# Optimization experiments

Measured on AMD Instinct MI355X. Metric: run time of the kernel, lower is better.

## Reference

```python
import jax, jax.numpy as jnp
import numpy as np

N = 50000      # nodes
E = 200000     # edges
F_IN = 128     # input features
H = 1024       # hidden
C = 16         # classes
K = 3          # TAGConv hops
EPS = 1e-5


def setup_inputs() -> dict:
    key = jax.random.key(0)
    ks = jax.random.split(key, 12)
    s = 0.02
    x = jax.random.normal(ks[0], (N, F_IN), jnp.float32)
    edge_index = jax.random.randint(ks[1], (2, E), 0, N, dtype=jnp.int64)
    weight = jax.random.uniform(ks[2], (E,), jnp.float32)
    return {
        "x": x,
        "edge_index": edge_index,
        "weight": weight,
        "W1": jax.random.normal(ks[3], (K + 1, F_IN, H), jnp.float32) * s,
        "b1": jnp.zeros((H,), jnp.float32),
        "g1": jnp.ones((H,), jnp.float32),
        "be1": jnp.zeros((H,), jnp.float32),
        "a1": jnp.ones((H,), jnp.float32),
        "W2": jax.random.normal(ks[4], (K + 1, H, H), jnp.float32) * s,
        "b2": jnp.zeros((H,), jnp.float32),
        "g2": jnp.ones((H,), jnp.float32),
        "be2": jnp.zeros((H,), jnp.float32),
        "a2": jnp.ones((H,), jnp.float32),
        "W3": jax.random.normal(ks[5], (K + 1, H, C), jnp.float32) * s,
        "b3": jnp.zeros((C,), jnp.float32),
    }


def _edge_norm(weight, src, dst):
    # gcn_norm without self-loops: deg from edge weights at target nodes
    deg = jax.ops.segment_sum(weight, dst, num_segments=N)
    safe = jnp.where(deg > 0, deg, 1.0)
    dinv = jnp.where(deg > 0, jax.lax.rsqrt(safe), 0.0)
    norm_w = dinv[src] * weight * dinv[dst]
    cnt = jax.ops.segment_sum(jnp.ones((E,), weight.dtype), dst, num_segments=N)
    cnt_inv = jnp.where(cnt > 0, 1.0 / jnp.where(cnt > 0, cnt, 1.0), 0.0)
    return norm_w, cnt_inv


def _tagconv(x, W, b, src, dst, norm_w, cnt_inv):
    # out = sum_k lin_k(x_k), x_k = mean-aggr of norm_w * x_{k-1}[src] at dst
    out = x @ W[0]
    h = x
    for k in range(1, K + 1):
        msg = norm_w[:, None] * h[src]                       # [E, d]
        h = jax.ops.segment_sum(msg, dst, num_segments=N) * cnt_inv[:, None]
        out = out + h @ W[k]
    return out + b


def _graphnorm(x, g, be, a):
    # single graph: per-graph stats = global stats over nodes
    mean = jnp.mean(x, axis=0)
    out = x - a * mean
    var = jnp.mean(out * out, axis=0)
    return g * out / jnp.sqrt(var + EPS) + be


def reference(x, edge_index, weight, W1, b1, g1, be1, a1,
              W2, b2, g2, be2, a2, W3, b3):
    src, dst = edge_index[0], edge_index[1]
    norm_w, cnt_inv = _edge_norm(weight, src, dst)
    h = jax.nn.elu(_tagconv(x, W1, b1, src, dst, norm_w, cnt_inv))
    h = _graphnorm(h, g1, be1, a1)
    h = jax.nn.elu(_tagconv(h, W2, b2, src, dst, norm_w, cnt_inv))
    h = _graphnorm(h, g2, be2, a2)
    return _tagconv(h, W3, b3, src, dst, norm_w, cnt_inv)
```

## Files before the change

kernel.cpp:

```cpp
#include <hip/hip_runtime.h>
#include <hip/hip_bf16.h>
#include <math.h>

#define N_NODES 50000
#define N_EDGES 200000
#define FIN 128
#define HID 1024
#define NCLS 16
#define EPSN 1e-5f
#define NPAD 50048
#define MT 391
#define EPITCH 136

typedef __attribute__((ext_vector_type(8))) short short8;
typedef __attribute__((ext_vector_type(8))) unsigned short ushort8;
typedef __attribute__((ext_vector_type(4))) unsigned short u16x4;
typedef __attribute__((ext_vector_type(4))) float f32x4;

static __device__ __forceinline__ float bf2f(unsigned short u) {
  union { unsigned int i; float f; } v; v.i = ((unsigned int)u) << 16; return v.f;
}
static __device__ __forceinline__ unsigned short f2bf(float f) {
  __hip_bfloat16 h = __float2bfloat16(f);
  return *(unsigned short*)&h;
}

#define ASYNC16(gsrc, ldst)                                                   \
  __builtin_amdgcn_global_load_lds(                                           \
      (const __attribute__((address_space(1))) void*)(gsrc),                  \
      (__attribute__((address_space(3))) void*)(ldst), 16, 0, 0)


__global__ __launch_bounds__(256) void k_deg_cnt(const int* __restrict__ dst,
                                                 const float* __restrict__ w,
                                                 float* deg, int* cnt) {
  int e = blockIdx.x * 256 + threadIdx.x;
  if (e < N_EDGES) {
    int d = dst[e];
    atomicAdd(&deg[d], w[e]);
    atomicAdd(&cnt[d], 1);
  }
}

__global__ __launch_bounds__(256) void k_normw(const int* __restrict__ src,
                                               const int* __restrict__ dst,
                                               const float* __restrict__ w,
                                               const float* __restrict__ deg,
                                               float* __restrict__ normw) {
  int e = blockIdx.x * 256 + threadIdx.x;
  if (e < N_EDGES) {
    float ds = deg[src[e]], dd = deg[dst[e]];
    float a = ds > 0.f ? rsqrtf(ds) : 0.f;
    float b = dd > 0.f ? rsqrtf(dd) : 0.f;
    normw[e] = a * w[e] * b;
  }
}

__global__ __launch_bounds__(256) void k_cntinv(const int* __restrict__ cnt,
                                                float* __restrict__ cnt_inv) {
  int n = blockIdx.x * 256 + threadIdx.x;
  if (n < N_NODES) {
    int c = cnt[n];
    cnt_inv[n] = c > 0 ? 1.f / (float)c : 0.f;
  }
}

__global__ __launch_bounds__(1024) void k_scan_a(const int* __restrict__ cnt,
                                                 int* __restrict__ rowptr,
                                                 int* __restrict__ bsums) {
  __shared__ int sm[1024];
  int tid = threadIdx.x;
  int i = blockIdx.x * 1024 + tid;
  int v = (i < N_NODES) ? cnt[i] : 0;
  sm[tid] = v;
  __syncthreads();
  for (int off = 1; off < 1024; off <<= 1) {
    int t = (tid >= off) ? sm[tid - off] : 0;
    __syncthreads();
    sm[tid] += t;
    __syncthreads();
  }
  if (i < N_NODES) rowptr[i] = sm[tid] - v;
  if (tid == 1023) bsums[blockIdx.x] = sm[1023];
}

__global__ void k_scan_b(int* bsums, int nb) {
  if (threadIdx.x == 0 && blockIdx.x == 0) {
    int s = 0;
    for (int i = 0; i < nb; ++i) { int t = bsums[i]; bsums[i] = s; s += t; }
  }
}

__global__ __launch_bounds__(1024) void k_scan_c(int* __restrict__ rowptr,
                                                 const int* __restrict__ bsums) {
  int i = blockIdx.x * 1024 + threadIdx.x;
  if (i < N_NODES) rowptr[i] += bsums[blockIdx.x];
}

__global__ __launch_bounds__(256) void k_fill(const int* __restrict__ src,
                                              const int* __restrict__ dst,
                                              const float* __restrict__ normw,
                                              const int* __restrict__ rowptr,
                                              int* __restrict__ fill,
                                              int* __restrict__ csr_src,
                                              float* __restrict__ csr_w) {
  int e = blockIdx.x * 256 + threadIdx.x;
  if (e < N_EDGES) {
    int d = dst[e];
    int pos = rowptr[d] + atomicAdd(&fill[d], 1);
    csr_src[pos] = src[e];
    csr_w[pos] = normw[e];
  }
}


__global__ void k_transpose_bf16(const float* __restrict__ in,
                                 __hip_bfloat16* __restrict__ out, int K, int N) {
  __shared__ float tile[32][33];
  int kb = blockIdx.x * 32, nb = blockIdx.y * 32;
  int tx = threadIdx.x, ty = threadIdx.y;
  for (int i = ty; i < 32; i += 8) tile[i][tx] = in[(size_t)(kb + i) * N + nb + tx];
  __syncthreads();
  for (int i = ty; i < 32; i += 8)
    out[(size_t)(nb + i) * K + kb + tx] = __float2bfloat16(tile[tx][i]);
}

__global__ __launch_bounds__(256) void k_packw3(const float* __restrict__ W3,
                                                __hip_bfloat16* __restrict__ W3T) {
  int idx = blockIdx.x * 256 + threadIdx.x;
  if (idx < 4 * 1024 * 16) {
    int k3 = idx >> 14, r = idx & 16383, k = r >> 4, j = r & 15;
    W3T[(size_t)(k3 * 16 + j) * 1024 + k] = __float2bfloat16(W3[idx]);
  }
}

__global__ __launch_bounds__(256) void k_x_to_bf16(const float* __restrict__ x,
                                                   unsigned short* __restrict__ xc) {
  int i = blockIdx.x * 256 + threadIdx.x;
  if (i < N_NODES * FIN / 4) {
    int n = i >> 5, c4 = i & 31;
    const float4 v = ((const float4*)x)[i];
    u16x4 o;
    o[0] = f2bf(v.x); o[1] = f2bf(v.y); o[2] = f2bf(v.z); o[3] = f2bf(v.w);
    *(u16x4*)&xc[(size_t)n * 512 + c4 * 4] = o;
  }
}


template <int W>
__global__ __launch_bounds__(256) void k_spmm_v(
    const unsigned short* __restrict__ src_t, int sp,
    unsigned short* __restrict__ dst_t, int dp,
    const int* __restrict__ rowptr, const int* __restrict__ cnt,
    const float* __restrict__ cnt_inv,
    const int* __restrict__ csr_src,
    const float* __restrict__ csr_w) {
  constexpr int G = W / 8;
  int gl = blockIdx.x * 256 + threadIdx.x;
  int node = gl / G;
  if (node >= N_NODES) return;
  int fl = (gl % G) * 8;
  int beg = rowptr[node], ne = cnt[node];
  float acc[8] = {0.f, 0.f, 0.f, 0.f, 0.f, 0.f, 0.f, 0.f};
  for (int i = 0; i < ne; ++i) {
    int s = csr_src[beg + i];
    float wt = csr_w[beg + i];
    ushort8 v = *(const ushort8*)&src_t[(size_t)s * sp + fl];
#pragma unroll
    for (int j = 0; j < 8; ++j) acc[j] += wt * bf2f(v[j]);
  }
  float ci = cnt_inv[node];
  ushort8 o;
#pragma unroll
  for (int j = 0; j < 8; ++j) o[j] = f2bf(acc[j] * ci);
  *(ushort8*)&dst_t[(size_t)node * dp + fl] = o;
}

__global__ __launch_bounds__(256) void k_spmm16(const float* __restrict__ src_t, int sp,
                                                const float* __restrict__ addend, int ap,
                                                const float* __restrict__ b3,
                                                float* __restrict__ out, int op,
                                                const int* __restrict__ rowptr,
                                                const int* __restrict__ cnt,
                                                const float* __restrict__ cnt_inv,
                                                const int* __restrict__ csr_src,
                                                const float* __restrict__ csr_w) {
  int idx = blockIdx.x * 256 + threadIdx.x;
  if (idx >= N_NODES * 16) return;
  int node = idx >> 4, f = idx & 15;
  int beg = rowptr[node], ne = cnt[node];
  float acc = 0.f;
  for (int i = 0; i < ne; ++i)
    acc += csr_w[beg + i] * src_t[(size_t)csr_src[beg + i] * sp + f];
  float r = acc * cnt_inv[node] + addend[(size_t)node * ap + f];
  if (b3) r += b3[f];
  out[(size_t)node * op + f] = r;
}


__global__ __launch_bounds__(256, 4) void k_gemm(
    const unsigned short* __restrict__ A, int lda,
    const unsigned short* __restrict__ BT, int ldb,
    const unsigned short* __restrict__ Cinit, int ldci,
    void* __restrict__ Cout, int ldc, int cbf16,
    int M, int Nout, int K,
    const float* __restrict__ bias, int do_elu) {
  __shared__ __align__(16) unsigned short smem[128 * EPITCH];
  int tid = threadIdx.x;
  int wave = tid >> 6, lane = tid & 63;
  int wm = wave >> 1, wn = wave & 1;
  int l15 = lane & 15, quad = lane >> 4;
  int im = blockIdx.y, in_ = blockIdx.x;

  f32x4 acc[4][4];
  if (Cinit) {
    {
      int r = tid >> 1, hf = tid & 1;
      const unsigned short* gsrc =
          &Cinit[(size_t)(im * 128 + r) * ldci + in_ * 128 + hf * 64];
#pragma unroll
      for (int v = 0; v < 8; ++v)
        *(ushort8*)&smem[r * EPITCH + hf * 64 + v * 8] = *(const ushort8*)&gsrc[v * 8];
    }
    __syncthreads();
#pragma unroll
    for (int i = 0; i < 4; ++i)
#pragma unroll
      for (int j = 0; j < 4; ++j)
#pragma unroll
        for (int reg = 0; reg < 4; ++reg)
          acc[i][j][reg] =
              bf2f(smem[(wm * 64 + i * 16 + quad * 4 + reg) * EPITCH + wn * 64 + j * 16 + l15]);
    __syncthreads();
  } else {
#pragma unroll
    for (int i = 0; i < 4; ++i)
#pragma unroll
      for (int j = 0; j < 4; ++j) acc[i][j] = (f32x4){0.f, 0.f, 0.f, 0.f};
  }

  int srow = tid >> 2;
  int sl = (tid & 3) ^ (srow & 3) ^ ((srow >> 2) & 3);
  const unsigned short* gA0 = &A[(size_t)(im * 128 + srow) * lda + sl * 8];
  const unsigned short* gA1 = &A[(size_t)(im * 128 + 64 + srow) * lda + sl * 8];
  const unsigned short* gB0 = &BT[(size_t)(in_ * 128 + srow) * ldb + sl * 8];
  const unsigned short* gB1 = &BT[(size_t)(in_ * 128 + 64 + srow) * ldb + sl * 8];
  unsigned short* ldsA = smem;
  unsigned short* ldsB = smem + 8192;
  int woff0 = (wave * 64) * 8;
  int woff1 = (256 + wave * 64) * 8;
  int rsl = (quad ^ (l15 & 3) ^ (l15 >> 2)) * 8;

  auto stage = [&](int k0, int p) {
    ASYNC16(gA0 + k0, &ldsA[p * 4096 + woff0]);
    ASYNC16(gA1 + k0, &ldsA[p * 4096 + woff1]);
    ASYNC16(gB0 + k0, &ldsB[p * 4096 + woff0]);
    ASYNC16(gB1 + k0, &ldsB[p * 4096 + woff1]);
  };
  auto compute = [&](int p) {
    short8 af[4], bf[4];
#pragma unroll
    for (int i = 0; i < 4; ++i)
      af[i] = *(const short8*)&ldsA[p * 4096 + (wm * 64 + i * 16 + l15) * 32 + rsl];
#pragma unroll
    for (int j = 0; j < 4; ++j)
      bf[j] = *(const short8*)&ldsB[p * 4096 + (wn * 64 + j * 16 + l15) * 32 + rsl];
#pragma unroll
    for (int i = 0; i < 4; ++i)
#pragma unroll
      for (int j = 0; j < 4; ++j)
        acc[i][j] = __builtin_amdgcn_mfma_f32_16x16x32_bf16(af[i], bf[j], acc[i][j], 0, 0, 0);
  };

  stage(0, 0);
  __syncthreads();
  int p = 0;
  for (int k0 = 32; k0 < K; k0 += 32) {
    stage(k0, p ^ 1);
    compute(p);
    __syncthreads();
    p ^= 1;
  }
  compute(p);
  __syncthreads();

  if (cbf16) {
#pragma unroll
    for (int i = 0; i < 4; ++i)
#pragma unroll
      for (int j = 0; j < 4; ++j) {
        int cg = in_ * 128 + wn * 64 + j * 16 + l15;
        float bv = bias ? bias[cg] : 0.f;
#pragma unroll
        for (int reg = 0; reg < 4; ++reg) {
          float v = acc[i][j][reg] + bv;
          if (do_elu) v = v > 0.f ? v : expm1f(v);
          smem[(wm * 64 + i * 16 + quad * 4 + reg) * EPITCH + wn * 64 + j * 16 + l15] = f2bf(v);
        }
      }
    __syncthreads();
    int r = tid >> 1, hf = tid & 1;
    unsigned short* gdst =
        (unsigned short*)Cout + (size_t)(im * 128 + r) * ldc + in_ * 128 + hf * 64;
#pragma unroll
    for (int v = 0; v < 8; ++v)
      *(ushort8*)&gdst[v * 8] = *(const ushort8*)&smem[r * EPITCH + hf * 64 + v * 8];
  } else {
#pragma unroll
    for (int i = 0; i < 4; ++i) {
      int r0 = im * 128 + wm * 64 + i * 16 + quad * 4;
#pragma unroll
      for (int j = 0; j < 4; ++j) {
        int c = in_ * 128 + wn * 64 + j * 16 + l15;
        if (c < Nout) {
#pragma unroll
          for (int reg = 0; reg < 4; ++reg) {
            int r = r0 + reg;
            if (r < M) {
              float v = acc[i][j][reg];
              if (bias) v += bias[c];
              if (do_elu) v = v > 0.f ? v : expm1f(v);
              ((float*)Cout)[(size_t)r * ldc + c] = v;
            }
          }
        }
      }
    }
  }
}


__global__ __launch_bounds__(128) void k_colstats(const unsigned short* __restrict__ h,
                                                  float* __restrict__ stats) {
  int f0 = threadIdx.x * 8;
  int r0 = blockIdx.y * 128;
  int r1 = r0 + 128; if (r1 > N_NODES) r1 = N_NODES;
  float s[8] = {0,0,0,0,0,0,0,0}, s2[8] = {0,0,0,0,0,0,0,0};
  for (int r = r0; r < r1; ++r) {
    ushort8 v = *(const ushort8*)&h[(size_t)r * HID + f0];
#pragma unroll
    for (int j = 0; j < 8; ++j) { float x = bf2f(v[j]); s[j] += x; s2[j] += x * x; }
  }
#pragma unroll
  for (int j = 0; j < 8; ++j) {
    atomicAdd(&stats[f0 + j], s[j]);
    atomicAdd(&stats[HID + f0 + j], s2[j]);
  }
}

__global__ __launch_bounds__(256) void k_finalize(const float* __restrict__ g,
                                                  const float* __restrict__ be,
                                                  const float* __restrict__ a,
                                                  float* __restrict__ stats) {
  int f = blockIdx.x * 256 + threadIdx.x;
  if (f < HID) {
    float m = stats[f] / (float)N_NODES;
    float ex2 = stats[HID + f] / (float)N_NODES;
    float av = a[f];
    float var = ex2 - 2.f * av * m * m + av * av * m * m;
    float alpha = g[f] * rsqrtf(var + EPSN);
    stats[2 * HID + f] = alpha;
    stats[3 * HID + f] = be[f] - alpha * av * m;
  }
}

__global__ __launch_bounds__(256) void k_normalize(unsigned short* __restrict__ h,
                                                   const float* __restrict__ stats) {
  int i = blockIdx.x * 256 + threadIdx.x;
  if (i < N_NODES * HID / 8) {
    int f0 = (i * 8) & 1023;
    ushort8 v = *(ushort8*)&h[(size_t)i * 8];
#pragma unroll
    for (int j = 0; j < 8; ++j)
      v[j] = f2bf(stats[2 * HID + f0 + j] * bf2f(v[j]) + stats[3 * HID + f0 + j]);
    *(ushort8*)&h[(size_t)i * 8] = v;
  }
}


extern "C" void kernel_launch(void* const* d_in, const int* in_sizes, int n_in,
                              void* d_out, int out_size, void* d_ws, size_t ws_size,
                              hipStream_t stream) {
  const float* x   = (const float*)d_in[0];
  const int*   ei  = (const int*)d_in[1];
  const float* w   = (const float*)d_in[2];
  const float* W1  = (const float*)d_in[3];
  const float* b1  = (const float*)d_in[4];
  const float* g1  = (const float*)d_in[5];
  const float* be1 = (const float*)d_in[6];
  const float* a1  = (const float*)d_in[7];
  const float* W2  = (const float*)d_in[8];
  const float* b2  = (const float*)d_in[9];
  const float* g2  = (const float*)d_in[10];
  const float* be2 = (const float*)d_in[11];
  const float* a2  = (const float*)d_in[12];
  const float* W3  = (const float*)d_in[13];
  const float* b3  = (const float*)d_in[14];
  float* out = (float*)d_out;

  const int* srcI = ei;
  const int* dstI = ei + N_EDGES;

  char* base = (char*)d_ws;
  size_t off = 0;
  auto alloc = [&](size_t bytes) -> char* {
    char* p = base + off;
    off += (bytes + 255) & ~(size_t)255;
    return p;
  };

  float* deg      = (float*)alloc(N_NODES * 4);
  int*   cnt      = (int*)alloc(N_NODES * 4);
  float* cnt_inv  = (float*)alloc(N_NODES * 4);
  float* normw    = (float*)alloc(N_EDGES * 4);
  int*   rowptr   = (int*)alloc((N_NODES + 1) * 4);
  int*   fill     = (int*)alloc(N_NODES * 4);
  int*   bsums    = (int*)alloc(64 * 4);
  int*   csr_src  = (int*)alloc(N_EDGES * 4);
  float* csr_w    = (float*)alloc(N_EDGES * 4);
  float* stats    = (float*)alloc(4 * HID * 4);
  __hip_bfloat16* W1T = (__hip_bfloat16*)alloc((size_t)1024 * 512 * 2);
  __hip_bfloat16* W2T = (__hip_bfloat16*)alloc((size_t)1024 * 4096 * 2);
  __hip_bfloat16* W3T = (__hip_bfloat16*)alloc((size_t)128 * 1024 * 2);
  const size_t FT = (size_t)NPAD * HID * 2;
  unsigned short* T0 = (unsigned short*)alloc(FT);
  unsigned short* T1 = (unsigned short*)alloc(FT);
  size_t rem = (ws_size > off) ? (ws_size - off) : 0;
  bool full = rem >= FT + 1024;
  unsigned short *T2 = nullptr, *Q = nullptr, *R = nullptr;
  int wcols = 0;
  if (full) {
    T2 = (unsigned short*)alloc(FT);
  } else {
    wcols = 512;
    if (rem < 2 * (size_t)NPAD * 512 * 2 + 1024) wcols = 256;
    if (wcols == 256 && rem < 2 * (size_t)NPAD * 256 * 2 + 1024) wcols = 128;
    Q = (unsigned short*)alloc((size_t)NPAD * wcols * 2);
    R = (unsigned short*)alloc((size_t)NPAD * wcols * 2);
  }
  float* Z  = (float*)T0;
  float* t0 = (float*)((char*)T0 + (size_t)16 * 1024 * 1024);
  float* t1 = (float*)((char*)T0 + (size_t)24 * 1024 * 1024);
  (void)n_in; (void)in_sizes; (void)out_size;

  const int EB = (N_EDGES + 255) / 256;
  const int NB = (N_NODES + 255) / 256;

  (void)hipMemsetAsync(deg, 0, N_NODES * 4, stream);
  (void)hipMemsetAsync(cnt, 0, N_NODES * 4, stream);
  (void)hipMemsetAsync(fill, 0, N_NODES * 4, stream);
  k_deg_cnt<<<EB, 256, 0, stream>>>(dstI, w, deg, cnt);
  k_normw<<<EB, 256, 0, stream>>>(srcI, dstI, w, deg, normw);
  k_cntinv<<<NB, 256, 0, stream>>>(cnt, cnt_inv);
  k_scan_a<<<49, 1024, 0, stream>>>(cnt, rowptr, bsums);
  k_scan_b<<<1, 64, 0, stream>>>(bsums, 49);
  k_scan_c<<<49, 1024, 0, stream>>>(rowptr, bsums);
  k_fill<<<EB, 256, 0, stream>>>(srcI, dstI, normw, rowptr, fill, csr_src, csr_w);

  k_transpose_bf16<<<dim3(512 / 32, 1024 / 32), dim3(32, 8), 0, stream>>>(W1, W1T, 512, 1024);
  k_transpose_bf16<<<dim3(4096 / 32, 1024 / 32), dim3(32, 8), 0, stream>>>(W2, W2T, 4096, 1024);
  k_packw3<<<(65536 + 255) / 256, 256, 0, stream>>>(W3, W3T);

  const unsigned short* W2Tu = (const unsigned short*)W2T;

  k_x_to_bf16<<<(N_NODES * FIN / 4 + 255) / 256, 256, 0, stream>>>(x, T1);
  {
    int blocks = (N_NODES * 16 + 255) / 256;
    for (int k = 1; k <= 3; ++k)
      k_spmm_v<128><<<blocks, 256, 0, stream>>>(
          T1 + (k - 1) * FIN, 512, T1 + k * FIN, 512,
          rowptr, cnt, cnt_inv, csr_src, csr_w);
  }
  k_gemm<<<dim3(8, MT), 256, 0, stream>>>(
      T1, 512, (const unsigned short*)W1T, 512,
      nullptr, 0, T0, HID, 1, N_NODES, HID, 512, b1, 1);
  (void)hipMemsetAsync(stats, 0, 2 * HID * 4, stream);
  k_colstats<<<dim3(1, MT), 128, 0, stream>>>(T0, stats);
  k_finalize<<<4, 256, 0, stream>>>(g1, be1, a1, stats);
  k_normalize<<<(N_NODES * HID / 8) / 256, 256, 0, stream>>>(T0, stats);

  if (full) {
    const int SPB = (N_NODES * 128 + 255) / 256;
    k_gemm<<<dim3(8, MT), 256, 0, stream>>>(
        T0, 1024, W2Tu + 3 * 1024, 4096,
        nullptr, 0, T1, 1024, 1, N_NODES, 1024, 1024, nullptr, 0);
    k_spmm_v<1024><<<SPB, 256, 0, stream>>>(T1, 1024, T2, 1024,
                                            rowptr, cnt, cnt_inv, csr_src, csr_w);
    k_gemm<<<dim3(8, MT), 256, 0, stream>>>(
        T0, 1024, W2Tu + 2 * 1024, 4096,
        T2, 1024, T1, 1024, 1, N_NODES, 1024, 1024, nullptr, 0);
    k_spmm_v<1024><<<SPB, 256, 0, stream>>>(T1, 1024, T2, 1024,
                                            rowptr, cnt, cnt_inv, csr_src, csr_w);
    k_gemm<<<dim3(8, MT), 256, 0, stream>>>(
        T0, 1024, W2Tu + 1 * 1024, 4096,
        T2, 1024, T1, 1024, 1, N_NODES, 1024, 1024, nullptr, 0);
    k_spmm_v<1024><<<SPB, 256, 0, stream>>>(T1, 1024, T2, 1024,
                                            rowptr, cnt, cnt_inv, csr_src, csr_w);
    k_gemm<<<dim3(8, MT), 256, 0, stream>>>(
        T0, 1024, W2Tu + 0 * 1024, 4096,
        T2, 1024, T1, 1024, 1, N_NODES, 1024, 1024, b2, 1);
  } else {
    auto spmm_w = [&](const unsigned short* s, unsigned short* d) {
      int blocks = (N_NODES * (wcols / 8) + 255) / 256;
      if (wcols == 512)
        k_spmm_v<512><<<blocks, 256, 0, stream>>>(s, wcols, d, wcols,
            rowptr, cnt, cnt_inv, csr_src, csr_w);
      else if (wcols == 256)
        k_spmm_v<256><<<blocks, 256, 0, stream>>>(s, wcols, d, wcols,
            rowptr, cnt, cnt_inv, csr_src, csr_w);
      else
        k_spmm_v<128><<<blocks, 256, 0, stream>>>(s, wcols, d, wcols,
            rowptr, cnt, cnt_inv, csr_src, csr_w);
    };
    for (int c = 0; c < HID; c += wcols) {
      const unsigned short* Wb = W2Tu + (size_t)c * 4096;
      k_gemm<<<dim3(wcols / 128, MT), 256, 0, stream>>>(
          T0, 1024, Wb + 3 * 1024, 4096,
          nullptr, 0, Q, wcols, 1, N_NODES, wcols, 1024, nullptr, 0);
      spmm_w(Q, R);
      k_gemm<<<dim3(wcols / 128, MT), 256, 0, stream>>>(
          T0, 1024, Wb + 2 * 1024, 4096,
          R, wcols, Q, wcols, 1, N_NODES, wcols, 1024, nullptr, 0);
      spmm_w(Q, R);
      k_gemm<<<dim3(wcols / 128, MT), 256, 0, stream>>>(
          T0, 1024, Wb + 1 * 1024, 4096,
          R, wcols, Q, wcols, 1, N_NODES, wcols, 1024, nullptr, 0);
      spmm_w(Q, R);
      k_gemm<<<dim3(wcols / 128, MT), 256, 0, stream>>>(
          T0, 1024, Wb + 0 * 1024, 4096,
          R, wcols, T1 + c, 1024, 1, N_NODES, wcols, 1024, b2 + c, 1);
    }
  }
  (void)hipMemsetAsync(stats, 0, 2 * HID * 4, stream);
  k_colstats<<<dim3(1, MT), 128, 0, stream>>>(T1, stats);
  k_finalize<<<4, 256, 0, stream>>>(g2, be2, a2, stats);
  k_normalize<<<(N_NODES * HID / 8) / 256, 256, 0, stream>>>(T1, stats);

  k_gemm<<<dim3(1, MT), 256, 0, stream>>>(
      T1, 1024, (const unsigned short*)W3T, 1024,
      nullptr, 0, Z, 64, 0, N_NODES, 64, 1024, nullptr, 0);
  const int SB = (N_NODES * 16 + 255) / 256;
  k_spmm16<<<SB, 256, 0, stream>>>(Z + 48, 64, Z + 32, 64, nullptr, t0, 16,
                                   rowptr, cnt, cnt_inv, csr_src, csr_w);
  k_spmm16<<<SB, 256, 0, stream>>>(t0, 16, Z + 16, 64, nullptr, t1, 16,
                                   rowptr, cnt, cnt_inv, csr_src, csr_w);
  k_spmm16<<<SB, 256, 0, stream>>>(t1, 16, Z + 0, 64, b3, out, 16,
                                   rowptr, cnt, cnt_inv, csr_src, csr_w);
}
```

Baseline: 2.107 ms.

## Fold first GraphNorm affine into layer-2 weights and per-hop bias vectors

Drops the explicit normalize pass over the 50000x1024 hidden activations after layer 1. The per-feature GraphNorm scale is folded into the transposed bf16 W2, and the shift is folded into per-hop bias vectors ck computed by a new small kernel, which the GEMM epilogues then add. This is valid because aggregation is linear, but it relies on finalize having written scale and shift into stats at offsets 2*HID and 3*HID. It also packs CSR source index and weight into one int2 array, and makes column statistics reduce through shared memory to cut global atomics.

```diff
diff --git a/kernel.cpp b/kernel.cpp
--- a/kernel.cpp
+++ b/kernel.cpp
@@ -102,14 +102,12 @@
                                               const float* __restrict__ normw,
                                               const int* __restrict__ rowptr,
                                               int* __restrict__ fill,
-                                              int* __restrict__ csr_src,
-                                              float* __restrict__ csr_w) {
+                                              int2* __restrict__ csr_ew) {
   int e = blockIdx.x * 256 + threadIdx.x;
   if (e < N_EDGES) {
     int d = dst[e];
     int pos = rowptr[d] + atomicAdd(&fill[d], 1);
-    csr_src[pos] = src[e];
-    csr_w[pos] = normw[e];
+    csr_ew[pos] = make_int2(src[e], __float_as_int(normw[e]));
   }
 }
 
@@ -125,6 +123,40 @@
     out[(size_t)(nb + i) * K + kb + tx] = __float2bfloat16(tile[tx][i]);
 }
 
+__global__ void k_transpose_scale_bf16(const float* __restrict__ in,
+                                       __hip_bfloat16* __restrict__ out, int K, int N,
+                                       const float* __restrict__ alpha) {
+  __shared__ float tile[32][33];
+  int kb = blockIdx.x * 32, nb = blockIdx.y * 32;
+  int tx = threadIdx.x, ty = threadIdx.y;
+  for (int i = ty; i < 32; i += 8) tile[i][tx] = in[(size_t)(kb + i) * N + nb + tx];
+  __syncthreads();
+  float sc = alpha[(kb + tx) & (HID - 1)];
+  for (int i = ty; i < 32; i += 8)
+    out[(size_t)(nb + i) * K + kb + tx] = __float2bfloat16(tile[tx][i] * sc);
+}
+
+__global__ __launch_bounds__(256) void k_ck(const float* __restrict__ W2,
+                                            const float* __restrict__ beta,
+                                            const float* __restrict__ b2,
+                                            float* __restrict__ ck) {
+  int k3 = blockIdx.x, tid = threadIdx.x;
+  float acc[4] = {0.f, 0.f, 0.f, 0.f};
+  const float* Wk = W2 + (size_t)k3 * HID * HID;
+  for (int in = 0; in < HID; ++in) {
+    float s = beta[in];
+    const float* row = Wk + (size_t)in * HID;
+#pragma unroll
+    for (int j = 0; j < 4; ++j) acc[j] += s * row[tid + j * 256];
+  }
+#pragma unroll
+  for (int j = 0; j < 4; ++j) {
+    float v = acc[j];
+    if (k3 == 0) v += b2[tid + j * 256];
+    ck[k3 * HID + tid + j * 256] = v;
+  }
+}
+
 __global__ __launch_bounds__(256) void k_packw3(const float* __restrict__ W3,
                                                 __hip_bfloat16* __restrict__ W3T) {
   int idx = blockIdx.x * 256 + threadIdx.x;
@@ -153,8 +185,7 @@
     unsigned short* __restrict__ dst_t, int dp,
     const int* __restrict__ rowptr, const int* __restrict__ cnt,
     const float* __restrict__ cnt_inv,
-    const int* __restrict__ csr_src,
-    const float* __restrict__ csr_w) {
+    const int2* __restrict__ csr_ew) {
   constexpr int G = W / 8;
   int gl = blockIdx.x * 256 + threadIdx.x;
   int node = gl / G;
@@ -163,9 +194,9 @@
   int beg = rowptr[node], ne = cnt[node];
   float acc[8] = {0.f, 0.f, 0.f, 0.f, 0.f, 0.f, 0.f, 0.f};
   for (int i = 0; i < ne; ++i) {
-    int s = csr_src[beg + i];
-    float wt = csr_w[beg + i];
-    ushort8 v = *(const ushort8*)&src_t[(size_t)s * sp + fl];
+    int2 e = csr_ew[beg + i];
+    float wt = __int_as_float(e.y);
+    ushort8 v = *(const ushort8*)&src_t[(size_t)e.x * sp + fl];
 #pragma unroll
     for (int j = 0; j < 8; ++j) acc[j] += wt * bf2f(v[j]);
   }
@@ -183,15 +214,16 @@
                                                 const int* __restrict__ rowptr,
                                                 const int* __restrict__ cnt,
                                                 const float* __restrict__ cnt_inv,
-                                                const int* __restrict__ csr_src,
-                                                const float* __restrict__ csr_w) {
+                                                const int2* __restrict__ csr_ew) {
   int idx = blockIdx.x * 256 + threadIdx.x;
   if (idx >= N_NODES * 16) return;
   int node = idx >> 4, f = idx & 15;
   int beg = rowptr[node], ne = cnt[node];
   float acc = 0.f;
-  for (int i = 0; i < ne; ++i)
-    acc += csr_w[beg + i] * src_t[(size_t)csr_src[beg + i] * sp + f];
+  for (int i = 0; i < ne; ++i) {
+    int2 e = csr_ew[beg + i];
+    acc += __int_as_float(e.y) * src_t[(size_t)e.x * sp + f];
+  }
   float r = acc * cnt_inv[node] + addend[(size_t)node * ap + f];
   if (b3) r += b3[f];
   out[(size_t)node * op + f] = r;
@@ -330,11 +362,14 @@
 }
 
 
-__global__ __launch_bounds__(128) void k_colstats(const unsigned short* __restrict__ h,
+__global__ __launch_bounds__(512) void k_colstats(const unsigned short* __restrict__ h,
                                                   float* __restrict__ stats) {
-  int f0 = threadIdx.x * 8;
-  int r0 = blockIdx.y * 128;
-  int r1 = r0 + 128; if (r1 > N_NODES) r1 = N_NODES;
+  __shared__ float sm[4 * 2048];
+  int tid = threadIdx.x;
+  int f0 = (tid & 127) * 8;
+  int q = tid >> 7;
+  int r0 = blockIdx.y * 128 + q * 32;
+  int r1 = r0 + 32; if (r1 > N_NODES) r1 = N_NODES;
   float s[8] = {0,0,0,0,0,0,0,0}, s2[8] = {0,0,0,0,0,0,0,0};
   for (int r = r0; r < r1; ++r) {
     ushort8 v = *(const ushort8*)&h[(size_t)r * HID + f0];
@@ -343,8 +378,13 @@
   }
 #pragma unroll
   for (int j = 0; j < 8; ++j) {
-    atomicAdd(&stats[f0 + j], s[j]);
-    atomicAdd(&stats[HID + f0 + j], s2[j]);
+    sm[q * 2048 + f0 + j] = s[j];
+    sm[q * 2048 + 1024 + f0 + j] = s2[j];
+  }
+  __syncthreads();
+  for (int idx = tid; idx < 2048; idx += 512) {
+    float v = sm[idx] + sm[2048 + idx] + sm[4096 + idx] + sm[6144 + idx];
+    atomicAdd(&stats[idx], v);
   }
 }
 
@@ -416,9 +456,9 @@
   int*   rowptr   = (int*)alloc((N_NODES + 1) * 4);
   int*   fill     = (int*)alloc(N_NODES * 4);
   int*   bsums    = (int*)alloc(64 * 4);
-  int*   csr_src  = (int*)alloc(N_EDGES * 4);
-  float* csr_w    = (float*)alloc(N_EDGES * 4);
+  int2*  csr_ew   = (int2*)alloc((size_t)N_EDGES * 8);
   float* stats    = (float*)alloc(4 * HID * 4);
+  float* ck       = (float*)alloc(4 * HID * 4);
   __hip_bfloat16* W1T = (__hip_bfloat16*)alloc((size_t)1024 * 512 * 2);
   __hip_bfloat16* W2T = (__hip_bfloat16*)alloc((size_t)1024 * 4096 * 2);
   __hip_bfloat16* W3T = (__hip_bfloat16*)alloc((size_t)128 * 1024 * 2);
@@ -455,10 +495,9 @@
   k_scan_a<<<49, 1024, 0, stream>>>(cnt, rowptr, bsums);
   k_scan_b<<<1, 64, 0, stream>>>(bsums, 49);
   k_scan_c<<<49, 1024, 0, stream>>>(rowptr, bsums);
-  k_fill<<<EB, 256, 0, stream>>>(srcI, dstI, normw, rowptr, fill, csr_src, csr_w);
+  k_fill<<<EB, 256, 0, stream>>>(srcI, dstI, normw, rowptr, fill, csr_ew);
 
   k_transpose_bf16<<<dim3(512 / 32, 1024 / 32), dim3(32, 8), 0, stream>>>(W1, W1T, 512, 1024);
-  k_transpose_bf16<<<dim3(4096 / 32, 1024 / 32), dim3(32, 8), 0, stream>>>(W2, W2T, 4096, 1024);
   k_packw3<<<(65536 + 255) / 256, 256, 0, stream>>>(W3, W3T);
 
   const unsigned short* W2Tu = (const unsigned short*)W2T;
@@ -469,70 +508,72 @@
     for (int k = 1; k <= 3; ++k)
       k_spmm_v<128><<<blocks, 256, 0, stream>>>(
           T1 + (k - 1) * FIN, 512, T1 + k * FIN, 512,
-          rowptr, cnt, cnt_inv, csr_src, csr_w);
+          rowptr, cnt, cnt_inv, csr_ew);
   }
   k_gemm<<<dim3(8, MT), 256, 0, stream>>>(
       T1, 512, (const unsigned short*)W1T, 512,
       nullptr, 0, T0, HID, 1, N_NODES, HID, 512, b1, 1);
   (void)hipMemsetAsync(stats, 0, 2 * HID * 4, stream);
-  k_colstats<<<dim3(1, MT), 128, 0, stream>>>(T0, stats);
+  k_colstats<<<dim3(1, MT), 512, 0, stream>>>(T0, stats);
   k_finalize<<<4, 256, 0, stream>>>(g1, be1, a1, stats);
-  k_normalize<<<(N_NODES * HID / 8) / 256, 256, 0, stream>>>(T0, stats);
+  k_transpose_scale_bf16<<<dim3(4096 / 32, 1024 / 32), dim3(32, 8), 0, stream>>>(
+      W2, W2T, 4096, 1024, stats + 2 * HID);
+  k_ck<<<4, 256, 0, stream>>>(W2, stats + 3 * HID, b2, ck);
 
   if (full) {
     const int SPB = (N_NODES * 128 + 255) / 256;
     k_gemm<<<dim3(8, MT), 256, 0, stream>>>(
         T0, 1024, W2Tu + 3 * 1024, 4096,
-        nullptr, 0, T1, 1024, 1, N_NODES, 1024, 1024, nullptr, 0);
+        nullptr, 0, T1, 1024, 1, N_NODES, 1024, 1024, ck + 3 * 1024, 0);
     k_spmm_v<1024><<<SPB, 256, 0, stream>>>(T1, 1024, T2, 1024,
-                                            rowptr, cnt, cnt_inv, csr_src, csr_w);
+                                            rowptr, cnt, cnt_inv, csr_ew);
     k_gemm<<<dim3(8, MT), 256, 0, stream>>>(
         T0, 1024, W2Tu + 2 * 1024, 4096,
-        T2, 1024, T1, 1024, 1, N_NODES, 1024, 1024, nullptr, 0);
+        T2, 1024, T1, 1024, 1, N_NODES, 1024, 1024, ck + 2 * 1024, 0);
     k_spmm_v<1024><<<SPB, 256, 0, stream>>>(T1, 1024, T2, 1024,
-                                            rowptr, cnt, cnt_inv, csr_src, csr_w);
+                                            rowptr, cnt, cnt_inv, csr_ew);
     k_gemm<<<dim3(8, MT), 256, 0, stream>>>(
         T0, 1024, W2Tu + 1 * 1024, 4096,
-        T2, 1024, T1, 1024, 1, N_NODES, 1024, 1024, nullptr, 0);
+        T2, 1024, T1, 1024, 1, N_NODES, 1024, 1024, ck + 1 * 1024, 0);
     k_spmm_v<1024><<<SPB, 256, 0, stream>>>(T1, 1024, T2, 1024,
-                                            rowptr, cnt, cnt_inv, csr_src, csr_w);
+                                            rowptr, cnt, cnt_inv, csr_ew);
     k_gemm<<<dim3(8, MT), 256, 0, stream>>>(
         T0, 1024, W2Tu + 0 * 1024, 4096,
-        T2, 1024, T1, 1024, 1, N_NODES, 1024, 1024, b2, 1);
+        T2, 1024, T1, 1024, 1, N_NODES, 1024, 1024, ck + 0 * 1024, 1);
   } else {
     auto spmm_w = [&](const unsigned short* s, unsigned short* d) {
       int blocks = (N_NODES * (wcols / 8) + 255) / 256;
       if (wcols == 512)
         k_spmm_v<512><<<blocks, 256, 0, stream>>>(s, wcols, d, wcols,
-            rowptr, cnt, cnt_inv, csr_src, csr_w);
+            rowptr, cnt, cnt_inv, csr_ew);
       else if (wcols == 256)
         k_spmm_v<256><<<blocks, 256, 0, stream>>>(s, wcols, d, wcols,
-            rowptr, cnt, cnt_inv, csr_src, csr_w);
+            rowptr, cnt, cnt_inv, csr_ew);
       else
         k_spmm_v<128><<<blocks, 256, 0, stream>>>(s, wcols, d, wcols,
-            rowptr, cnt, cnt_inv, csr_src, csr_w);
+            rowptr, cnt, cnt_inv, csr_ew);
     };
     for (int c = 0; c < HID; c += wcols) {
       const unsigned short* Wb = W2Tu + (size_t)c * 4096;
       k_gemm<<<dim3(wcols / 128, MT), 256, 0, stream>>>(
           T0, 1024, Wb + 3 * 1024, 4096,
-          nullptr, 0, Q, wcols, 1, N_NODES, wcols, 1024, nullptr, 0);
+          nullptr, 0, Q, wcols, 1, N_NODES, wcols, 1024, ck + 3 * 1024 + c, 0);
       spmm_w(Q, R);
       k_gemm<<<dim3(wcols / 128, MT), 256, 0, stream>>>(
           T0, 1024, Wb + 2 * 1024, 4096,
-          R, wcols, Q, wcols, 1, N_NODES, wcols, 1024, nullptr, 0);
+          R, wcols, Q, wcols, 1, N_NODES, wcols, 1024, ck + 2 * 1024 + c, 0);
       spmm_w(Q, R);
       k_gemm<<<dim3(wcols / 128, MT), 256, 0, stream>>>(
           T0, 1024, Wb + 1 * 1024, 4096,
-          R, wcols, Q, wcols, 1, N_NODES, wcols, 1024, nullptr, 0);
+          R, wcols, Q, wcols, 1, N_NODES, wcols, 1024, ck + 1 * 1024 + c, 0);
       spmm_w(Q, R);
       k_gemm<<<dim3(wcols / 128, MT), 256, 0, stream>>>(
           T0, 1024, Wb + 0 * 1024, 4096,
-          R, wcols, T1 + c, 1024, 1, N_NODES, wcols, 1024, b2 + c, 1);
+          R, wcols, T1 + c, 1024, 1, N_NODES, wcols, 1024, ck + 0 * 1024 + c, 1);
     }
   }
   (void)hipMemsetAsync(stats, 0, 2 * HID * 4, stream);
-  k_colstats<<<dim3(1, MT), 128, 0, stream>>>(T1, stats);
+  k_colstats<<<dim3(1, MT), 512, 0, stream>>>(T1, stats);
   k_finalize<<<4, 256, 0, stream>>>(g2, be2, a2, stats);
   k_normalize<<<(N_NODES * HID / 8) / 256, 256, 0, stream>>>(T1, stats);
 
@@ -541,9 +582,9 @@
       nullptr, 0, Z, 64, 0, N_NODES, 64, 1024, nullptr, 0);
   const int SB = (N_NODES * 16 + 255) / 256;
   k_spmm16<<<SB, 256, 0, stream>>>(Z + 48, 64, Z + 32, 64, nullptr, t0, 16,
-                                   rowptr, cnt, cnt_inv, csr_src, csr_w);
+                                   rowptr, cnt, cnt_inv, csr_ew);
   k_spmm16<<<SB, 256, 0, stream>>>(t0, 16, Z + 16, 64, nullptr, t1, 16,
-                                   rowptr, cnt, cnt_inv, csr_src, csr_w);
+                                   rowptr, cnt, cnt_inv, csr_ew);
   k_spmm16<<<SB, 256, 0, stream>>>(t1, 16, Z + 0, 64, b3, out, 16,
-                                   rowptr, cnt, cnt_inv, csr_src, csr_w);
-}
+                                   rowptr, cnt, cnt_inv, csr_ew);
+}
```

Result: faster. 1.978 ms (-6.1%).
